# Optimization experiments

Hardware: AMD Instinct MI355X
Metric: run time of the kernel (lower is better)

## Reference

```python
import jax, jax.numpy as jnp
import numpy as np

N_NODES = 25000
N_EDGES = 400000
D = 1024


def setup_inputs() -> dict:
    key = jax.random.key(0)
    ks = jax.random.split(key, 8)
    s = 1.0 / np.sqrt(D)
    return {
        "x": jax.random.normal(ks[0], (N_NODES, D), dtype=jnp.float32),
        "edge_src": jax.random.randint(ks[1], (N_EDGES,), 0, N_NODES, dtype=jnp.int32),
        "edge_dst": jax.random.randint(ks[2], (N_EDGES,), 0, N_NODES, dtype=jnp.int32),
        "W_self0": jax.random.normal(ks[3], (D, D), dtype=jnp.float32) * s,
        "W_neigh0": jax.random.normal(ks[4], (D, D), dtype=jnp.float32) * s,
        "b0": jnp.zeros((D,), dtype=jnp.float32),
        "W_self1": jax.random.normal(ks[5], (D, D), dtype=jnp.float32) * s,
        "W_neigh1": jax.random.normal(ks[6], (D, D), dtype=jnp.float32) * s,
        "b1": jnp.zeros((D,), dtype=jnp.float32),
    }


def _sage_layer(h, edge_src, edge_dst, deg_inv, W_self, W_neigh, b):
    # mean aggregation over in-neighbors: gather src feats, segment-sum by dst
    msg = h[edge_src]                                            # [E, d]
    agg = jax.ops.segment_sum(msg, edge_dst, num_segments=h.shape[0])  # [N, d]
    mean = agg * deg_inv[:, None]
    return h @ W_self + mean @ W_neigh + b


def reference(x, edge_src, edge_dst, W_self0, W_neigh0, b0, W_self1, W_neigh1, b1):
    N = x.shape[0]
    deg = jax.ops.segment_sum(jnp.ones_like(edge_dst, dtype=x.dtype), edge_dst, num_segments=N)
    deg_inv = 1.0 / jnp.maximum(deg, 1.0)  # isolated nodes -> 0 neighbor mean
    h = jax.nn.relu(_sage_layer(x, edge_src, edge_dst, deg_inv, W_self0, W_neigh0, b0))
    out = _sage_layer(h, edge_src, edge_dst, deg_inv, W_self1, W_neigh1, b1)
    return out
```

## Files before the change

kernel.cpp:

```cpp
#include <hip/hip_runtime.h>
#include <stdint.h>

#define NN 25000
#define NE 400000
#define DD 1024

typedef __attribute__((ext_vector_type(8))) short short8;
typedef __attribute__((ext_vector_type(4))) float f32x4;

__device__ __forceinline__ unsigned short f2bf(float f) {
  union { float f; uint32_t u; } v; v.f = f;
  uint32_t r = v.u + 0x7fffu + ((v.u >> 16) & 1u);
  return (unsigned short)(r >> 16);
}
__device__ __forceinline__ float bf2f(unsigned short h) {
  union { uint32_t u; float f; } v; v.u = ((uint32_t)h) << 16;
  return v.f;
}

__device__ __forceinline__ void gld_lds16(const void* g, void* l) {
  __builtin_amdgcn_global_load_lds(
      (const __attribute__((address_space(1))) void*)g,
      (__attribute__((address_space(3))) void*)l, 16, 0, 0);
}

__global__ __launch_bounds__(256) void k_cast_bf16(const float* __restrict__ in,
                                                   unsigned short* __restrict__ out,
                                                   int n8) {
  int i = blockIdx.x * blockDim.x + threadIdx.x;
  int stride = gridDim.x * blockDim.x;
  for (; i < n8; i += stride) {
    const float4* p = (const float4*)(in + (size_t)i * 8);
    float4 a = p[0], b = p[1];
    ushort4 r0, r1;
    r0.x = f2bf(a.x); r0.y = f2bf(a.y); r0.z = f2bf(a.z); r0.w = f2bf(a.w);
    r1.x = f2bf(b.x); r1.y = f2bf(b.y); r1.z = f2bf(b.z); r1.w = f2bf(b.w);
    ushort4* q = (ushort4*)(out + (size_t)i * 8);
    q[0] = r0; q[1] = r1;
  }
}

__global__ __launch_bounds__(256) void k_transcast(const float* __restrict__ W,
                                                   unsigned short* __restrict__ WT,
                                                   int kofs) {
  __shared__ unsigned short tile[64][66];
  int t = threadIdx.x;
  int k0 = blockIdx.x * 64, n0 = blockIdx.y * 64;
#pragma unroll
  for (int p = 0; p < 16; ++p) {
    int idx = p * 256 + t;
    int lr = idx >> 6, lc = idx & 63;
    tile[lr][lc] = f2bf(W[(size_t)(k0 + lr) * 1024 + n0 + lc]);
  }
  __syncthreads();
#pragma unroll
  for (int p = 0; p < 16; ++p) {
    int idx = p * 256 + t;
    int lr = idx >> 6, lc = idx & 63;
    WT[(size_t)(n0 + lr) * 2048 + kofs + k0 + lc] = tile[lc][lr];
  }
}

__global__ __launch_bounds__(256) void k_deg(const int* __restrict__ dst,
                                             int* __restrict__ deg, int E) {
  int i = blockIdx.x * blockDim.x + threadIdx.x;
  if (i < E) atomicAdd(&deg[dst[i]], 1);
}

__global__ __launch_bounds__(256) void k_scan1(const int* __restrict__ deg,
                                               int* __restrict__ rowptr,
                                               int* __restrict__ bsum, int N) {
  __shared__ int ws[4];
  int t = threadIdx.x, lane = t & 63, w = t >> 6;
  int i = blockIdx.x * 256 + t;
  int v = (i < N) ? deg[i] : 0;
  int x = v;
#pragma unroll
  for (int off = 1; off < 64; off <<= 1) {
    int y = __shfl_up(x, off);
    if (lane >= off) x += y;
  }
  if (lane == 63) ws[w] = x;
  __syncthreads();
  int wbase = 0;
#pragma unroll
  for (int j = 0; j < 3; ++j)
    if (w > j) wbase += ws[j];
  if (i < N) rowptr[i] = wbase + x - v;
  if (t == 255) bsum[blockIdx.x] = wbase + x;
}

__global__ __launch_bounds__(128) void k_scan2(const int* __restrict__ bsum,
                                               int* __restrict__ boff,
                                               int* __restrict__ rowptr_end, int nb) {
  __shared__ int ws[2];
  int t = threadIdx.x, lane = t & 63, w = t >> 6;
  int v = (t < nb) ? bsum[t] : 0;
  int x = v;
#pragma unroll
  for (int off = 1; off < 64; off <<= 1) {
    int y = __shfl_up(x, off);
    if (lane >= off) x += y;
  }
  if (lane == 63) ws[w] = x;
  __syncthreads();
  int wbase = (w == 1) ? ws[0] : 0;
  if (t < nb) boff[t] = wbase + x - v;
  if (t == 127) *rowptr_end = wbase + x;
}

__global__ __launch_bounds__(256) void k_scan3(const int* __restrict__ deg,
                                               const int* __restrict__ boff,
                                               int* __restrict__ rowptr,
                                               int* __restrict__ cursor,
                                               float* __restrict__ dinv, int N) {
  int i = blockIdx.x * 256 + threadIdx.x;
  if (i < N) {
    int r = rowptr[i] + boff[blockIdx.x];
    rowptr[i] = r;
    cursor[i] = r;
    dinv[i] = 1.0f / fmaxf((float)deg[i], 1.0f);
  }
}

__global__ __launch_bounds__(256) void k_fill(const int* __restrict__ src,
                                              const int* __restrict__ dst,
                                              int* __restrict__ cursor,
                                              int* __restrict__ srcs, int E) {
  int i = blockIdx.x * blockDim.x + threadIdx.x;
  if (i < E) {
    int p = atomicAdd(&cursor[dst[i]], 1);
    srcs[p] = src[i];
  }
}

__global__ __launch_bounds__(256) void k_agg(const unsigned short* __restrict__ h,
                                             const int* __restrict__ rowptr,
                                             const int* __restrict__ srcs,
                                             const float* __restrict__ deg_inv,
                                             unsigned short* __restrict__ mean, int N) {
  int node = blockIdx.x * 2 + (threadIdx.x >> 7);
  if (node >= N) return;
  int t = threadIdx.x & 127;
  int c = t * 8;
  int beg = rowptr[node], end = rowptr[node + 1];
  float a[8];
#pragma unroll
  for (int j = 0; j < 8; ++j) a[j] = 0.f;
  int e = beg;
  for (; e + 1 < end; e += 2) {
    int s0 = srcs[e], s1 = srcs[e + 1];
    short8 v0 = *(const short8*)(h + (size_t)s0 * DD + c);
    short8 v1 = *(const short8*)(h + (size_t)s1 * DD + c);
#pragma unroll
    for (int j = 0; j < 8; ++j)
      a[j] += bf2f((unsigned short)v0[j]) + bf2f((unsigned short)v1[j]);
  }
  if (e < end) {
    int s0 = srcs[e];
    short8 v0 = *(const short8*)(h + (size_t)s0 * DD + c);
#pragma unroll
    for (int j = 0; j < 8; ++j) a[j] += bf2f((unsigned short)v0[j]);
  }
  float di = deg_inv[node];
  short8 r;
#pragma unroll
  for (int j = 0; j < 8; ++j) r[j] = (short)f2bf(a[j] * di);
  *(short8*)(mean + (size_t)node * DD + c) = r;
}

template <bool RELU, bool OUT_BF16>
__global__ __launch_bounds__(256) void k_gemm(const unsigned short* __restrict__ A1,
                                              const unsigned short* __restrict__ A2,
                                              const unsigned short* __restrict__ WT,
                                              const float* __restrict__ bias,
                                              void* __restrict__ Cout, int M) {
  __shared__ __align__(16) unsigned short lA[2][128 * 32];
  __shared__ __align__(16) unsigned short lB[2][128 * 32];
  const int t = threadIdx.x;
  const int lane = t & 63, wave = t >> 6;
  const int wm = wave >> 1, wn = wave & 1;
  const int fr = lane & 15, fq = lane >> 4;

  const int nbm = gridDim.x >> 3;
  const int hw = blockIdx.x;
  const int g = (hw & 7) * nbm + (hw >> 3);
  const int bm = g >> 3, bn = g & 7;

  f32x4 acc[4][4];
#pragma unroll
  for (int m = 0; m < 4; ++m)
#pragma unroll
    for (int n = 0; n < 4; ++n) acc[m][n] = (f32x4){0.f, 0.f, 0.f, 0.f};

  const int srow = t >> 2;
  const int skk = (t & 3) * 8;
  int ar0 = bm * 128 + srow;
  int ar1 = ar0 + 64;
  if (ar0 > M - 1) ar0 = M - 1;
  if (ar1 > M - 1) ar1 = M - 1;
  const int br0 = bn * 128 + srow;
  const int br1 = br0 + 64;

  auto stage = [&](int kt, int buf) {
    const unsigned short* As = (kt < 32) ? A1 : A2;
    const int ka = (kt & 31) * 32 + skk;
    const int kw = kt * 32 + skk;
    unsigned short* dA = &lA[buf][wave * 512];
    unsigned short* dB = &lB[buf][wave * 512];
    gld_lds16(As + (size_t)ar0 * 1024 + ka, dA);
    gld_lds16(As + (size_t)ar1 * 1024 + ka, dA + 2048);
    gld_lds16(WT + (size_t)br0 * 2048 + kw, dB);
    gld_lds16(WT + (size_t)br1 * 2048 + kw, dB + 2048);
  };

  stage(0, 0);
  __syncthreads();
  int cur = 0;
#pragma unroll 2
  for (int kt = 0; kt < 64; ++kt) {
    if (kt < 63) stage(kt + 1, cur ^ 1);
    short8 af[4], bfv[4];
#pragma unroll
    for (int m = 0; m < 4; ++m)
      af[m] = *(const short8*)&lA[cur][(wm * 64 + m * 16 + fr) * 32 + fq * 8];
#pragma unroll
    for (int n = 0; n < 4; ++n)
      bfv[n] = *(const short8*)&lB[cur][(wn * 64 + n * 16 + fr) * 32 + fq * 8];
#pragma unroll
    for (int m = 0; m < 4; ++m)
#pragma unroll
      for (int n = 0; n < 4; ++n)
        acc[m][n] = __builtin_amdgcn_mfma_f32_16x16x32_bf16(af[m], bfv[n], acc[m][n], 0, 0, 0);
    __syncthreads();
    cur ^= 1;
  }

#pragma unroll
  for (int m = 0; m < 4; ++m) {
    int r0 = bm * 128 + wm * 64 + m * 16 + fq * 4;
#pragma unroll
    for (int j = 0; j < 4; ++j) {
      int r = r0 + j;
      if (r >= M) continue;
#pragma unroll
      for (int n = 0; n < 4; ++n) {
        int cc = bn * 128 + wn * 64 + n * 16 + fr;
        float v = acc[m][n][j] + bias[cc];
        if (RELU) v = fmaxf(v, 0.f);
        if (OUT_BF16)
          ((unsigned short*)Cout)[(size_t)r * 1024 + cc] = f2bf(v);
        else
          ((float*)Cout)[(size_t)r * 1024 + cc] = v;
      }
    }
  }
}

extern "C" void kernel_launch(void* const* d_in, const int* in_sizes, int n_in,
                              void* d_out, int out_size, void* d_ws, size_t ws_size,
                              hipStream_t stream) {
  const float* x = (const float*)d_in[0];
  const int* esrc = (const int*)d_in[1];
  const int* edst = (const int*)d_in[2];
  const float* Ws0 = (const float*)d_in[3];
  const float* Wn0 = (const float*)d_in[4];
  const float* b0 = (const float*)d_in[5];
  const float* Ws1 = (const float*)d_in[6];
  const float* Wn1 = (const float*)d_in[7];
  const float* b1 = (const float*)d_in[8];
  float* out = (float*)d_out;

  char* ws = (char*)d_ws;
  size_t off = 0;
  auto alloc = [&](size_t bytes) -> void* {
    void* p = ws + off;
    off = (off + bytes + 255) & ~(size_t)255;
    return p;
  };
  unsigned short* x_bf = (unsigned short*)alloc((size_t)NN * DD * 2);
  unsigned short* h_bf = (unsigned short*)alloc((size_t)NN * DD * 2);
  unsigned short* mean_bf = (unsigned short*)alloc((size_t)NN * DD * 2);
  unsigned short* WT0 = (unsigned short*)alloc((size_t)DD * 2048 * 2);
  unsigned short* WT1 = (unsigned short*)alloc((size_t)DD * 2048 * 2);
  int* deg = (int*)alloc((size_t)NN * 4);
  int* rowptr = (int*)alloc((size_t)(NN + 1) * 4);
  int* cursor = (int*)alloc((size_t)NN * 4);
  float* dinv = (float*)alloc((size_t)NN * 4);
  int* srcs = (int*)alloc((size_t)NE * 4);
  int* bsum = (int*)alloc(128 * 4);
  int* boff = (int*)alloc(128 * 4);

  hipMemsetAsync(deg, 0, (size_t)NN * 4, stream);

  k_cast_bf16<<<2048, 256, 0, stream>>>(x, x_bf, NN * DD / 8);
  dim3 tg(16, 16);
  k_transcast<<<tg, 256, 0, stream>>>(Ws0, WT0, 0);
  k_transcast<<<tg, 256, 0, stream>>>(Wn0, WT0, 1024);
  k_transcast<<<tg, 256, 0, stream>>>(Ws1, WT1, 0);
  k_transcast<<<tg, 256, 0, stream>>>(Wn1, WT1, 1024);

  const int nsb = (NN + 255) / 256;
  k_deg<<<(NE + 255) / 256, 256, 0, stream>>>(edst, deg, NE);
  k_scan1<<<nsb, 256, 0, stream>>>(deg, rowptr, bsum, NN);
  k_scan2<<<1, 128, 0, stream>>>(bsum, boff, rowptr + NN, nsb);
  k_scan3<<<nsb, 256, 0, stream>>>(deg, boff, rowptr, cursor, dinv, NN);
  k_fill<<<(NE + 255) / 256, 256, 0, stream>>>(esrc, edst, cursor, srcs, NE);

  const int nbm = (NN + 127) / 128;
  dim3 gg(8 * nbm);

  k_agg<<<(NN + 1) / 2, 256, 0, stream>>>(x_bf, rowptr, srcs, dinv, mean_bf, NN);
  k_gemm<true, true><<<gg, 256, 0, stream>>>(x_bf, mean_bf, WT0, b0, (void*)h_bf, NN);

  k_agg<<<(NN + 1) / 2, 256, 0, stream>>>(h_bf, rowptr, srcs, dinv, mean_bf, NN);
  k_gemm<false, false><<<gg, 256, 0, stream>>>(h_bf, mean_bf, WT1, b1, (void*)out, NN);
}
```

Baseline: 786.7 us.

## Enlarge GEMM tiles to 256x256 with 8 waves and phased LDS pipeline

Rewrites the bf16 MFMA GEMM to use 256x256 output tiles with 512 threads, a 64-wide K step, and a 128KB double-buffered LDS area with an XOR swizzle. Each K step is split into four compute phases. Prefetch of the next tile's halves is interleaved between the phases, and setprio is raised around the MFMA bursts. The aim is higher arithmetic intensity per byte loaded, fewer LDS bank conflicts and better overlap of global-to-LDS loads with compute. In exchange, occupancy is limited to one large block per CU, register pressure is higher (32 accumulators per wave), and the 98x4 grid may leave CUs idle at the tail.

```diff
diff --git a/kernel.cpp b/kernel.cpp
--- a/kernel.cpp
+++ b/kernel.cpp
@@ -170,88 +170,127 @@
 }
 
 template <bool RELU, bool OUT_BF16>
-__global__ __launch_bounds__(256) void k_gemm(const unsigned short* __restrict__ A1,
-                                              const unsigned short* __restrict__ A2,
-                                              const unsigned short* __restrict__ WT,
-                                              const float* __restrict__ bias,
-                                              void* __restrict__ Cout, int M) {
-  __shared__ __align__(16) unsigned short lA[2][128 * 32];
-  __shared__ __align__(16) unsigned short lB[2][128 * 32];
+__global__ __launch_bounds__(512, 2) void k_gemm(const unsigned short* __restrict__ A1,
+                                                 const unsigned short* __restrict__ A2,
+                                                 const unsigned short* __restrict__ WT,
+                                                 const float* __restrict__ bias,
+                                                 void* __restrict__ Cout, int M) {
+  __shared__ __align__(16) char ldsc[131072];
   const int t = threadIdx.x;
   const int lane = t & 63, wave = t >> 6;
-  const int wm = wave >> 1, wn = wave & 1;
+  const int wm = wave >> 2, wn = wave & 3;
   const int fr = lane & 15, fq = lane >> 4;
 
-  const int nbm = gridDim.x >> 3;
-  const int hw = blockIdx.x;
-  const int g = (hw & 7) * nbm + (hw >> 3);
-  const int bm = g >> 3, bn = g & 7;
-
-  f32x4 acc[4][4];
-#pragma unroll
-  for (int m = 0; m < 4; ++m)
+  const int cpx = gridDim.x >> 3;
+  const int g = (blockIdx.x & 7) * cpx + (blockIdx.x >> 3);
+  const int bm = g >> 2, bn = g & 3;
+
+  int sb = lane * 16;
+  sb ^= ((sb >> 9) & 1) << 5;
+  const int s_r = sb >> 6;
+  const int s_k = (sb & 63) >> 1;
+
+  int rd = fr * 64 + fq * 16;
+  rd ^= ((rd >> 9) & 1) << 5;
+
+  f32x4 acc[8][4];
+#pragma unroll
+  for (int m = 0; m < 8; ++m)
 #pragma unroll
     for (int n = 0; n < 4; ++n) acc[m][n] = (f32x4){0.f, 0.f, 0.f, 0.f};
 
-  const int srow = t >> 2;
-  const int skk = (t & 3) * 8;
-  int ar0 = bm * 128 + srow;
-  int ar1 = ar0 + 64;
-  if (ar0 > M - 1) ar0 = M - 1;
-  if (ar1 > M - 1) ar1 = M - 1;
-  const int br0 = bn * 128 + srow;
-  const int br1 = br0 + 64;
-
-  auto stage = [&](int kt, int buf) {
-    const unsigned short* As = (kt < 32) ? A1 : A2;
-    const int ka = (kt & 31) * 32 + skk;
-    const int kw = kt * 32 + skk;
-    unsigned short* dA = &lA[buf][wave * 512];
-    unsigned short* dB = &lB[buf][wave * 512];
-    gld_lds16(As + (size_t)ar0 * 1024 + ka, dA);
-    gld_lds16(As + (size_t)ar1 * 1024 + ka, dA + 2048);
-    gld_lds16(WT + (size_t)br0 * 2048 + kw, dB);
-    gld_lds16(WT + (size_t)br1 * 2048 + kw, dB + 2048);
+  auto stage_half = [&](int t1, int hi, int bufb) {
+    const bool isA = hi < 2;
+    const int half = hi & 1;
+    const unsigned short* src;
+    int stride, kb, row0;
+    if (isA) {
+      src = (t1 < 16) ? A1 : A2;
+      stride = 1024;
+      kb = (t1 & 15) * 64;
+      row0 = bm * 256 + half * 128;
+    } else {
+      src = WT;
+      stride = 2048;
+      kb = t1 * 64;
+      row0 = bn * 256 + half * 128;
+    }
+    char* lbase = ldsc + bufb + hi * 16384 + wave * 1024;
+#pragma unroll
+    for (int j = 0; j < 2; ++j) {
+      int sub = j * 8 + wave;
+      int msub = sub >> 1, ksub = sub & 1;
+      int row = row0 + msub * 16 + s_r;
+      if (isA && row > M - 1) row = M - 1;
+      gld_lds16(src + (size_t)row * stride + kb + ksub * 32 + s_k, lbase + j * 8192);
+    }
   };
 
-  stage(0, 0);
-  __syncthreads();
-  int cur = 0;
-#pragma unroll 2
-  for (int kt = 0; kt < 64; ++kt) {
-    if (kt < 63) stage(kt + 1, cur ^ 1);
-    short8 af[4], bfv[4];
-#pragma unroll
-    for (int m = 0; m < 4; ++m)
-      af[m] = *(const short8*)&lA[cur][(wm * 64 + m * 16 + fr) * 32 + fq * 8];
-#pragma unroll
-    for (int n = 0; n < 4; ++n)
-      bfv[n] = *(const short8*)&lB[cur][(wn * 64 + n * 16 + fr) * 32 + fq * 8];
-#pragma unroll
-    for (int m = 0; m < 4; ++m)
-#pragma unroll
-      for (int n = 0; n < 4; ++n)
-        acc[m][n] = __builtin_amdgcn_mfma_f32_16x16x32_bf16(af[m], bfv[n], acc[m][n], 0, 0, 0);
-    __syncthreads();
-    cur ^= 1;
-  }
-
-#pragma unroll
-  for (int m = 0; m < 4; ++m) {
-    int r0 = bm * 128 + wm * 64 + m * 16 + fq * 4;
+#define PHASE(QM, QN, STAGE)                                                          \
+  {                                                                                   \
+    short8 av[4][2], bv[2][2];                                                        \
+    _Pragma("unroll") for (int im = 0; im < 4; ++im)                                  \
+        _Pragma("unroll") for (int ks = 0; ks < 2; ++ks)                              \
+            av[im][ks] = *(const short8*)(pa + (((QM) * 4 + im) * 2 + ks) * 1024);    \
+    _Pragma("unroll") for (int in = 0; in < 2; ++in)                                  \
+        _Pragma("unroll") for (int ks = 0; ks < 2; ++ks)                              \
+            bv[in][ks] = *(const short8*)(pb + (((QN) * 2 + in) * 2 + ks) * 1024);    \
+    STAGE;                                                                            \
+    __builtin_amdgcn_s_barrier();                                                     \
+    __builtin_amdgcn_s_setprio(1);                                                    \
+    _Pragma("unroll") for (int im = 0; im < 4; ++im)                                  \
+        _Pragma("unroll") for (int in = 0; in < 2; ++in)                              \
+            _Pragma("unroll") for (int ks = 0; ks < 2; ++ks)                          \
+                acc[(QM) * 4 + im][(QN) * 2 + in] =                                   \
+                    __builtin_amdgcn_mfma_f32_16x16x32_bf16(                          \
+                        av[im][ks], bv[in][ks], acc[(QM) * 4 + im][(QN) * 2 + in],    \
+                        0, 0, 0);                                                     \
+    __builtin_amdgcn_s_setprio(0);                                                    \
+  }
+
+  stage_half(0, 0, 0);
+  stage_half(0, 1, 0);
+  stage_half(0, 2, 0);
+  stage_half(0, 3, 0);
+  asm volatile("s_waitcnt vmcnt(0)" ::: "memory");
+  __builtin_amdgcn_s_barrier();
+
+#pragma unroll 1
+  for (int kt = 0; kt < 32; ++kt) {
+    const int cbuf = (kt & 1) << 16;
+    const int nbuf = cbuf ^ 65536;
+    const bool pf = kt < 31;
+    const char* pa = ldsc + cbuf + wm * 16384 + rd;
+    const char* pb = ldsc + cbuf + 32768 + (wn >> 1) * 16384 + (wn & 1) * 8192 + rd;
+
+    PHASE(0, 0, if (pf) { stage_half(kt + 1, 0, nbuf); stage_half(kt + 1, 1, nbuf); })
+    __builtin_amdgcn_s_barrier();
+    PHASE(0, 1, if (pf) stage_half(kt + 1, 2, nbuf);)
+    __builtin_amdgcn_s_barrier();
+    PHASE(1, 0, if (pf) stage_half(kt + 1, 3, nbuf);)
+    __builtin_amdgcn_s_barrier();
+    PHASE(1, 1, ;)
+    asm volatile("s_waitcnt vmcnt(0)" ::: "memory");
+    __builtin_amdgcn_s_barrier();
+  }
+#undef PHASE
+
+#pragma unroll
+  for (int mf = 0; mf < 8; ++mf) {
+    int r0 = bm * 256 + wm * 128 + mf * 16 + fq * 4;
 #pragma unroll
     for (int j = 0; j < 4; ++j) {
       int r = r0 + j;
       if (r >= M) continue;
 #pragma unroll
-      for (int n = 0; n < 4; ++n) {
-        int cc = bn * 128 + wn * 64 + n * 16 + fr;
-        float v = acc[m][n][j] + bias[cc];
+      for (int nf = 0; nf < 4; ++nf) {
+        int c = bn * 256 + wn * 64 + nf * 16 + fr;
+        float v = acc[mf][nf][j] + bias[c];
         if (RELU) v = fmaxf(v, 0.f);
         if (OUT_BF16)
-          ((unsigned short*)Cout)[(size_t)r * 1024 + cc] = f2bf(v);
+          ((unsigned short*)Cout)[(size_t)r * 1024 + c] = f2bf(v);
         else
-          ((float*)Cout)[(size_t)r * 1024 + cc] = v;
+          ((float*)Cout)[(size_t)r * 1024 + c] = v;
       }
     }
   }
@@ -307,12 +346,12 @@
   k_scan3<<<nsb, 256, 0, stream>>>(deg, boff, rowptr, cursor, dinv, NN);
   k_fill<<<(NE + 255) / 256, 256, 0, stream>>>(esrc, edst, cursor, srcs, NE);
 
-  const int nbm = (NN + 127) / 128;
-  dim3 gg(8 * nbm);
+  const int nbm = (NN + 255) / 256;
+  dim3 gg(nbm * 4);
 
   k_agg<<<(NN + 1) / 2, 256, 0, stream>>>(x_bf, rowptr, srcs, dinv, mean_bf, NN);
-  k_gemm<true, true><<<gg, 256, 0, stream>>>(x_bf, mean_bf, WT0, b0, (void*)h_bf, NN);
+  k_gemm<true, true><<<gg, 512, 0, stream>>>(x_bf, mean_bf, WT0, b0, (void*)h_bf, NN);
 
   k_agg<<<(NN + 1) / 2, 256, 0, stream>>>(h_bf, rowptr, srcs, dinv, mean_bf, NN);
-  k_gemm<false, false><<<gg, 256, 0, stream>>>(h_bf, mean_bf, WT1, b1, (void*)out, NN);
-}
+  k_gemm<false, false><<<gg, 512, 0, stream>>>(h_bf, mean_bf, WT1, b1, (void*)out, NN);
+}
```

After: 749.3 us. -4.8%, faster.
